# Kernel optimization log

Measured on AMD Instinct MI355X. Metric: run time of the kernel, lower is better.

Reference implementation:

```python
import jax, jax.numpy as jnp
import numpy as np
from jax import lax

MASK_ID = 0  # sequence_mask pad token

def setup_inputs() -> dict:
    key = jax.random.key(0)
    ks = jax.random.split(key, 7)
    B, T, V, E, U_, O = 256, 128, 10000, 256, 1024, 1024
    return {
        "sequences": jax.random.randint(ks[0], (B, T), 0, V),
        "emb_table": jax.random.normal(ks[1], (V, E), jnp.float32) * 0.02,
        "W": jax.random.normal(ks[2], (E, 4 * U_), jnp.float32) * (1.0 / np.sqrt(E)),
        "U": jax.random.normal(ks[3], (U_, 4 * U_), jnp.float32) * (1.0 / np.sqrt(U_)),
        "b": jnp.zeros((4 * U_,), jnp.float32),
        "fc_W": jax.random.normal(ks[4], (U_, O), jnp.float32) * (1.0 / np.sqrt(U_)),
        "fc_b": jnp.zeros((O,), jnp.float32),
    }

def reference(sequences, emb_table, W, U, b, fc_W, fc_b):
    B, T = sequences.shape
    units = U.shape[0]
    # sequence_length_fn: count of non-pad tokens per row
    lengths = jnp.sum(sequences != MASK_ID, axis=1)  # [B]
    x = emb_table[sequences]                          # [B,T,E]
    # precompute input-to-gate contribution (fuses gate matmuls across time)
    x_gates = jnp.einsum('bte,eg->btg', x, W) + b     # [B,T,4U]
    valid = (jnp.arange(T)[:, None] < lengths[None, :])  # [T,B]

    def step(carry, inp):
        h, c = carry
        xg, v = inp                                   # [B,4U], [B]
        z = xg + h @ U
        i, f, g, o = jnp.split(z, 4, axis=-1)         # keras gate order i,f,c,o
        i = jax.nn.sigmoid(i)
        f = jax.nn.sigmoid(f)
        o = jax.nn.sigmoid(o)
        g = jnp.tanh(g)
        c_new = f * c + i * g
        h_new = o * jnp.tanh(c_new)
        vm = v[:, None]
        # dynamic_rnn: zero output past length, carry state through
        h_out = jnp.where(vm, h_new, 0.0)
        return (jnp.where(vm, h_new, h), jnp.where(vm, c_new, c)), h_out

    init = (jnp.zeros((B, units), x.dtype), jnp.zeros((B, units), x.dtype))
    _, outs = lax.scan(step, init, (jnp.swapaxes(x_gates, 0, 1), valid))
    outputs = jnp.swapaxes(outs, 0, 1)                # [B,T,U]
    return outputs @ fc_W + fc_b                      # [B,T,O]
```

## Files before the change

kernel.cpp:

```cpp
#include <hip/hip_runtime.h>

typedef short bf16x8 __attribute__((ext_vector_type(8)));
typedef float f32x4  __attribute__((ext_vector_type(4)));
typedef int   i32x4  __attribute__((ext_vector_type(4)));

#define DEVINL __device__ __forceinline__

static constexpr size_t SZ_WIM  = 4096ull * 512 * 2;
static constexpr size_t SZ_FCW  = 1024ull * 2048 * 2;
static constexpr size_t SZ_UIM  = 8388608;
static constexpr size_t SZ_EBI  = 10000ull * 512 * 2;
static constexpr size_t SZ_HH   = 33ull * 524288;
static constexpr size_t SZ_CB   = 1048576;
static constexpr size_t SZ_LEN  = 4096;
static constexpr size_t SZ_DIAG = 2048;

DEVINL unsigned short bf16rn(float x){
  unsigned u = __float_as_uint(x);
  unsigned r = (u + 0x7fffu + ((u >> 16) & 1u)) >> 16;
  return (unsigned short)r;
}
DEVINL unsigned short bf16lo(float x){
  unsigned ub = __float_as_uint(x);
  return bf16rn(x - __uint_as_float(ub & 0xffff0000u));
}
DEVINL float sigm(float x){ return 1.f / (1.f + __expf(-x)); }
DEVINL float tanhfast(float x){
  float xc = fminf(15.f, fmaxf(-15.f, x));
  float e = __expf(2.f * xc);
  return (e - 1.f) / (e + 1.f);
}
DEVINL void gl_lds16(const void* g, void* l){
  __builtin_amdgcn_global_load_lds(
      (const __attribute__((address_space(1))) unsigned*)g,
      (__attribute__((address_space(3))) unsigned*)l, 16, 0, 0);
}
DEVINL int hslot(int t){ return t % 33; }

__global__ void __launch_bounds__(256) probe_fill(float* __restrict__ out, int n, float v)
{
  int i = blockIdx.x * 256 + threadIdx.x;
  if (i < n) out[i] = (i == 0) ? v : 0.f;
}

__global__ void __launch_bounds__(64) diag_check(const int* __restrict__ prog,
                                                 float* __restrict__ out)
{
  if (threadIdx.x == 0){
    int miss = 0;
    for (int i = 7; i >= 1; i--) if (prog[i] == 0) miss = i;
    if (miss){
      for (int k = 0; k < 1024; k++) out[k] = 100.0f + (float)miss;
    }
  }
}

__global__ void __launch_bounds__(128) len_kernel(const int* __restrict__ seq,
                                                  int* __restrict__ len,
                                                  int* __restrict__ prog)
{
  int b = blockIdx.x, t = threadIdx.x;
  if (b == 0 && t == 0) prog[1] = 1;
  int pred = (seq[b * 128 + t] != 0) ? 1 : 0;
  unsigned long long m = __ballot(pred);
  __shared__ int cnt[2];
  if ((t & 63) == 0) cnt[t >> 6] = __popcll(m);
  __syncthreads();
  if (t == 0) len[b] = cnt[0] + cnt[1];
}

__global__ void __launch_bounds__(256) prep_split_img(
    const float* __restrict__ S, unsigned short* __restrict__ img, int N, int Ksrc,
    int* __restrict__ prog, int stage)
{
  __shared__ float tile[64][65];
  const int nt = N >> 6;
  const int bn = blockIdx.x % nt, bk = blockIdx.x / nt;
  const int tid = threadIdx.x;
  if (blockIdx.x == 0 && tid == 0) prog[stage] = 1;
  {
    const int kk = tid >> 6, n = tid & 63;
#pragma unroll 4
    for (int i = 0; i < 16; i++){
      int k = i * 4 + kk;
      tile[k][n] = S[(size_t)((bk << 6) + k) * N + (bn << 6) + n];
    }
  }
  __syncthreads();
  {
    const int n4 = tid >> 6, k = tid & 63;
#pragma unroll 4
    for (int i = 0; i < 16; i++){
      int n = i * 4 + n4;
      float v = tile[k][n];
      size_t rowoff = (size_t)((bn << 6) + n) * (2 * Ksrc) + (bk << 6) + k;
      img[rowoff] = (unsigned short)(__float_as_uint(v) >> 16);
      img[rowoff + Ksrc] = bf16lo(v);
    }
  }
}

__global__ void __launch_bounds__(256) prep_emb_img(const float* __restrict__ emb,
                                                    unsigned short* __restrict__ img)
{
  const int v = blockIdx.x, t = threadIdx.x;
  float x = emb[(size_t)v * 256 + t];
  img[(size_t)v * 512 + t]       = (unsigned short)(__float_as_uint(x) >> 16);
  img[(size_t)v * 512 + 256 + t] = bf16lo(x);
}

__global__ void __launch_bounds__(256) prep_uimg(const float* __restrict__ U,
                                                 signed char* __restrict__ img,
                                                 int* __restrict__ prog)
{
  const int bid = blockIdx.x;
  const int nb = bid >> 2, nt4 = bid & 3;
  const int tid = threadIdx.x;
  if (bid == 0 && tid == 0) prog[4] = 1;
  __shared__ signed char lc[16384], ldq[16384];
  const int colbase = nt4 * 1024 + (nb << 4);
  const int kk = tid >> 4, cc = tid & 15;
#pragma unroll 4
  for (int it = 0; it < 64; it++){
    int k = it * 16 + kk;
    float v = U[(size_t)k * 4096 + colbase + cc];
    int q = (int)rintf(v * 131072.f);
    q = q > 32639 ? 32639 : (q < -32639 ? -32639 : q);
    int a = (q + 128) >> 8;
    int d = q - (a << 8);
    lc[(k << 4) + cc]  = (signed char)a;
    ldq[(k << 4) + cc] = (signed char)d;
  }
  __syncthreads();
#pragma unroll
  for (int rep = 0; rep < 4; rep++){
    int idx = rep * 256 + tid;
    int kt = idx >> 6, lane = idx & 63;
    int n = lane & 15, quad = lane >> 4;
    union { signed char b[16]; i32x4 v; } cb_, db_;
#pragma unroll
    for (int j = 0; j < 16; j++){
      int k = (kt << 6) + (quad << 4) + j;
      cb_.b[j] = lc[(k << 4) + n];
      db_.b[j] = ldq[(k << 4) + n];
    }
    size_t base = (size_t)((((nb << 2) + nt4) * 16 + kt) * 2) * 1024;
    *(i32x4*)(img + base + (size_t)lane * 16)        = cb_.v;
    *(i32x4*)(img + base + 1024 + (size_t)lane * 16) = db_.v;
  }
}

__global__ void __launch_bounds__(256) gemm_gates(
    const unsigned short* __restrict__ Aimg, const unsigned short* __restrict__ Bimg,
    const float* __restrict__ bias, float* __restrict__ D,
    const int* __restrict__ seq, int c0, int tcsh, int* __restrict__ prog)
{
  __shared__ __align__(16) char lds[16384];
  __shared__ int stok[128];
  const int tid = threadIdx.x, lane = tid & 63, wv = tid >> 6;
  const int quad = lane >> 4, nlo = lane & 15;
  const int wm = wv & 1, wn = wv >> 1;
  const int rowbase = (blockIdx.x >> 5) << 7;
  const int colbase = (blockIdx.x & 31) << 7;
  const int tcm1 = (1 << tcsh) - 1;
  if (blockIdx.x == 0 && tid == 0) prog[5] = 1;
  if (tid < 128){
    int r = rowbase + tid;
    stok[tid] = seq[((r >> tcsh) << 7) + c0 + (r & tcm1)];
  }
  __syncthreads();

  f32x4 acc[4][4];
#pragma unroll
  for (int i = 0; i < 4; i++)
#pragma unroll
    for (int j = 0; j < 4; j++) acc[i][j] = (f32x4){0.f, 0.f, 0.f, 0.f};

  const unsigned short* asrc[2]; const unsigned short* bsrc[2];
  char* adst[2]; char* bdst[2];
#pragma unroll
  for (int p = 0; p < 2; p++){
    int gidx = p * 256 + tid;
    int row = gidx >> 2, sg = gidx & 3;
    int sgs = sg ^ ((row >> 1) & 3);
    asrc[p] = Aimg + (size_t)stok[row] * 512 + sgs * 8;
    bsrc[p] = Bimg + (size_t)(colbase + row) * 512 + sgs * 8;
    adst[p] = &lds[p * 4096 + wv * 1024];
    bdst[p] = &lds[8192 + p * 4096 + wv * 1024];
  }

#pragma unroll 2
  for (int c = 0; c < 24; c++){
    int k0 = c * 32;
    int seg = (k0 >= 512) ? 2 : (k0 >= 256 ? 1 : 0);
    int acol = k0 - seg * 256;
    int aoff = (seg == 1 ? 256 : 0) + acol;
    int boff = (seg == 2 ? 256 : 0) + acol;
    __syncthreads();
#pragma unroll
    for (int p = 0; p < 2; p++){
      gl_lds16(asrc[p] + aoff, adst[p]);
      gl_lds16(bsrc[p] + boff, bdst[p]);
    }
    __syncthreads();
    bf16x8 af[4], bfr[4];
#pragma unroll
    for (int mt = 0; mt < 4; mt++){
      int r = wm * 64 + mt * 16 + nlo;
      af[mt] = *(const bf16x8*)(&lds[r * 64 + ((quad ^ ((r >> 1) & 3)) << 4)]);
    }
#pragma unroll
    for (int nt = 0; nt < 4; nt++){
      int r = wn * 64 + nt * 16 + nlo;
      bfr[nt] = *(const bf16x8*)(&lds[8192 + r * 64 + ((quad ^ ((r >> 1) & 3)) << 4)]);
    }
#pragma unroll
    for (int mt = 0; mt < 4; mt++)
#pragma unroll
      for (int nt = 0; nt < 4; nt++)
        acc[mt][nt] = __builtin_amdgcn_mfma_f32_16x16x32_bf16(af[mt], bfr[nt], acc[mt][nt], 0, 0, 0);
  }

  float bs[4];
#pragma unroll
  for (int nt = 0; nt < 4; nt++) bs[nt] = bias[colbase + wn * 64 + nt * 16 + nlo];
#pragma unroll
  for (int mt = 0; mt < 4; mt++)
#pragma unroll
    for (int nt = 0; nt < 4; nt++){
      int col = colbase + wn * 64 + nt * 16 + nlo;
#pragma unroll
      for (int r = 0; r < 4; r++){
        int row = rowbase + wm * 64 + mt * 16 + quad * 4 + r;
        D[(size_t)row * 4096 + col] = acc[mt][nt][r] + bs[nt];
      }
    }
}

__global__ void __launch_bounds__(256) gemm_out(
    const unsigned short* __restrict__ ohol, const unsigned short* __restrict__ Bimg,
    const float* __restrict__ bias, float* __restrict__ D,
    int c0, int tcsh, int* __restrict__ prog)
{
  __shared__ __align__(16) char lds[16384];
  const int tid = threadIdx.x, lane = tid & 63, wv = tid >> 6;
  const int quad = lane >> 4, nlo = lane & 15;
  const int wm = wv & 1, wn = wv >> 1;
  const int rowbase = (blockIdx.x >> 3) << 7;
  const int colbase = (blockIdx.x & 7) << 7;
  const int tcm1 = (1 << tcsh) - 1;
  if (blockIdx.x == 0 && tid == 0) prog[7] = 1;

  f32x4 acc[4][4];
#pragma unroll
  for (int i = 0; i < 4; i++)
#pragma unroll
    for (int j = 0; j < 4; j++) acc[i][j] = (f32x4){0.f, 0.f, 0.f, 0.f};

  const unsigned short* asrc[2]; const unsigned short* bsrc[2];
  char* adst[2]; char* bdst[2];
#pragma unroll
  for (int p = 0; p < 2; p++){
    int gidx = p * 256 + tid;
    int row = gidx >> 2, sg = gidx & 3;
    int sgs = sg ^ ((row >> 1) & 3);
    asrc[p] = ohol + (size_t)(rowbase + row) * 2048 + sgs * 8;
    bsrc[p] = Bimg + (size_t)(colbase + row) * 2048 + sgs * 8;
    adst[p] = &lds[p * 4096 + wv * 1024];
    bdst[p] = &lds[8192 + p * 4096 + wv * 1024];
  }

#pragma unroll 2
  for (int c = 0; c < 96; c++){
    int k0 = c * 32;
    int seg = (k0 >= 2048) ? 2 : (k0 >= 1024 ? 1 : 0);
    int acol = k0 - seg * 1024;
    int aoff = (seg == 1 ? 1024 : 0) + acol;
    int boff = (seg == 2 ? 1024 : 0) + acol;
    __syncthreads();
#pragma unroll
    for (int p = 0; p < 2; p++){
      gl_lds16(asrc[p] + aoff, adst[p]);
      gl_lds16(bsrc[p] + boff, bdst[p]);
    }
    __syncthreads();
    bf16x8 af[4], bfr[4];
#pragma unroll
    for (int mt = 0; mt < 4; mt++){
      int r = wm * 64 + mt * 16 + nlo;
      af[mt] = *(const bf16x8*)(&lds[r * 64 + ((quad ^ ((r >> 1) & 3)) << 4)]);
    }
#pragma unroll
    for (int nt = 0; nt < 4; nt++){
      int r = wn * 64 + nt * 16 + nlo;
      bfr[nt] = *(const bf16x8*)(&lds[8192 + r * 64 + ((quad ^ ((r >> 1) & 3)) << 4)]);
    }
#pragma unroll
    for (int mt = 0; mt < 4; mt++)
#pragma unroll
      for (int nt = 0; nt < 4; nt++)
        acc[mt][nt] = __builtin_amdgcn_mfma_f32_16x16x32_bf16(af[mt], bfr[nt], acc[mt][nt], 0, 0, 0);
  }

  float bs[4];
#pragma unroll
  for (int nt = 0; nt < 4; nt++) bs[nt] = bias[colbase + wn * 64 + nt * 16 + nlo];
#pragma unroll
  for (int mt = 0; mt < 4; mt++)
#pragma unroll
    for (int nt = 0; nt < 4; nt++){
      int col = colbase + wn * 64 + nt * 16 + nlo;
#pragma unroll
      for (int r = 0; r < 4; r++){
        int row = rowbase + wm * 64 + mt * 16 + quad * 4 + r;
        int drow = ((row >> tcsh) << 7) + c0 + (row & tcm1);
        D[(size_t)drow * 1024 + col] = acc[mt][nt][r] + bs[nt];
      }
    }
}

DEVINL void mbbar(int* flags, int nb, int t, int wv, int lane){
  __syncthreads();
  if (wv == 0){
    if (lane == 0)
      __hip_atomic_store(&flags[nb], t + 1, __ATOMIC_RELAXED, __HIP_MEMORY_SCOPE_AGENT);
    const int tgt = t + 1;
    for (;;){
      int v = __hip_atomic_load(&flags[lane], __ATOMIC_RELAXED, __HIP_MEMORY_SCOPE_AGENT);
      if (__ballot(v >= tgt) == ~0ull) break;
      __builtin_amdgcn_s_sleep(1);
    }
    __builtin_amdgcn_fence(__ATOMIC_ACQUIRE, "workgroup");
  }
  __syncthreads();
}

__global__ void __launch_bounds__(512, 2) lstm_rec(
    const float* __restrict__ xg,
    const signed char* __restrict__ uimg,
    const int* __restrict__ len,
    signed char* __restrict__ hh,
    float* __restrict__ cbuf,
    unsigned short* __restrict__ ohol,
    int* __restrict__ barbase,
    int* __restrict__ prog,
    int c0, int tcsh)
{
  __shared__ __align__(16) char lds[50176];
  const int tc = 1 << tcsh;
  const int wg = blockIdx.x, mb = wg >> 6, nb = wg & 63;
  const int tid = threadIdx.x, lane = tid & 63, wv = tid >> 6;
  const int quad = lane >> 4, nlo = lane & 15;
  const int mh = wv & 1, g = wv >> 1;
  int* flags = barbase + (mb << 6);
  if (wg == 0 && tid == 0) prog[6] = 1;

  const unsigned short* hh2 = (const unsigned short*)hh;

  i32x4 Bf[16][2];
#pragma unroll
  for (int kt = 0; kt < 16; kt++)
#pragma unroll
    for (int pl = 0; pl < 2; pl++){
      size_t off = (size_t)((((nb << 2) + g) * 16 + kt) * 2 + pl);
      off = (off * 64 + lane) << 4;
      Bf[kt][pl] = *(const i32x4*)(uimg + off);
    }

  const int erow = tid >> 3;
  const int ecp  = tid & 7;
  const int ecol0 = ecp << 1;
  const int ucol0 = (nb << 4) + ecol0;
  const int bglob = (mb << 6) + erow;
  const int lenr = len[bglob];
  float cst[2], hst[2];
#pragma unroll
  for (int r = 0; r < 2; r++){
    cst[r] = cbuf[(size_t)bglob * 1024 + ucol0 + r];
    unsigned short e = hh2[(size_t)hslot(c0) * 262144 + (size_t)bglob * 1024 + ucol0 + r];
    int a = (signed char)(e >> 8), b_ = (signed char)(e & 255);
    hst[r] = (float)(a * 256 + b_) * (1.0f / 32512.0f);
  }

  float4 xreg[2];
  auto load_x = [&](int s){
#pragma unroll
    for (int it = 0; it < 2; it++){
      int idx = it * 512 + tid;
      int row = idx >> 4, c4 = idx & 15;
      xreg[it] = *(const float4*)(xg + (size_t)((((mb << 6) + row) << tcsh) + s) * 4096
                                  + (c4 >> 2) * 1024 + (nb << 4) + ((c4 & 3) << 2));
    }
  };
  load_x(0);

  const int hrw = tid >> 3, hsub = tid & 7;

#pragma unroll 1
  for (int s = 0; s < tc; s++){
    const int t = c0 + s;
    const signed char* hsrc = hh + (size_t)hslot(t) * 524288 + (size_t)(mb << 6) * 2048;

    i32x4 accH[2], accM[2], accL[2];
#pragma unroll
    for (int m = 0; m < 2; m++){
      accH[m] = (i32x4){0,0,0,0};
      accM[m] = (i32x4){0,0,0,0};
      accL[m] = (i32x4){0,0,0,0};
    }

    int4 hregA[2], hregB[2];
    auto load_hto = [&](int c, int4* dst){
      const signed char* p = hsrc + (size_t)hrw * 2048 + c * 256 + hsub * 32;
      dst[0] = *(const int4*)p;
      dst[1] = *(const int4*)(p + 16);
    };
    auto write_hf = [&](const int4* src){
      unsigned r0 = (unsigned)src[0].x, r1 = (unsigned)src[0].y;
      unsigned r2 = (unsigned)src[0].z, r3 = (unsigned)src[0].w;
      unsigned r4 = (unsigned)src[1].x, r5 = (unsigned)src[1].y;
      unsigned r6 = (unsigned)src[1].z, r7 = (unsigned)src[1].w;
      i32x4 lo, hi;
      lo[0] = __builtin_amdgcn_perm(r1, r0, 0x06040200u);
      lo[1] = __builtin_amdgcn_perm(r3, r2, 0x06040200u);
      lo[2] = __builtin_amdgcn_perm(r5, r4, 0x06040200u);
      lo[3] = __builtin_amdgcn_perm(r7, r6, 0x06040200u);
      hi[0] = __builtin_amdgcn_perm(r1, r0, 0x07050301u);
      hi[1] = __builtin_amdgcn_perm(r3, r2, 0x07050301u);
      hi[2] = __builtin_amdgcn_perm(r5, r4, 0x07050301u);
      hi[3] = __builtin_amdgcn_perm(r7, r6, 0x07050301u);
      int sw = (hsub ^ (hrw & 7)) << 4;
      *(i32x4*)(&lds[hrw * 128 + sw])        = hi;
      *(i32x4*)(&lds[8192 + hrw * 128 + sw]) = lo;
    };

    load_hto(0, hregA);
    load_hto(1, hregB);

#pragma unroll
    for (int c = 0; c < 8; c++){
      __syncthreads();
      if ((c & 1) == 0) write_hf(hregA); else write_hf(hregB);
      if (c == 0){
#pragma unroll
        for (int it = 0; it < 2; it++){
          int idx = it * 512 + tid;
          int row = idx >> 4, c4 = idx & 15;
          *(float4*)(&lds[16384 + row * 256 + c4 * 16]) = xreg[it];
        }
      }
      __syncthreads();
      if (c + 2 < 8){
        if ((c & 1) == 0) load_hto(c + 2, hregA); else load_hto(c + 2, hregB);
      }
#pragma unroll
      for (int kt2 = 0; kt2 < 2; kt2++){
        const int kt = c * 2 + kt2;
        i32x4 Af[2][2];
#pragma unroll
        for (int m = 0; m < 2; m++){
          int hrow = (mh << 5) + (m << 4) + nlo;
          int sgl = ((kt2 << 2) + quad) ^ (hrow & 7);
          Af[m][0] = *(const i32x4*)(&lds[hrow * 128 + (sgl << 4)]);
          Af[m][1] = *(const i32x4*)(&lds[8192 + hrow * 128 + (sgl << 4)]);
        }
#pragma unroll
        for (int m = 0; m < 2; m++){
          accH[m] = __builtin_amdgcn_mfma_i32_16x16x64_i8(Af[m][0], Bf[kt][0], accH[m], 0, 0, 0);
          accM[m] = __builtin_amdgcn_mfma_i32_16x16x64_i8(Af[m][0], Bf[kt][1], accM[m], 0, 0, 0);
          accM[m] = __builtin_amdgcn_mfma_i32_16x16x64_i8(Af[m][1], Bf[kt][0], accM[m], 0, 0, 0);
          accL[m] = __builtin_amdgcn_mfma_i32_16x16x64_i8(Af[m][1], Bf[kt][1], accL[m], 0, 0, 0);
        }
      }
    }
    __syncthreads();

    if (s + 1 < tc) load_x(s + 1);

    const float cH = 1.0f / 65024.0f;
    const float cM = 1.0f / 16646144.0f;
    const float cL = 1.0f / 4261412864.0f;
#pragma unroll
    for (int m = 0; m < 2; m++){
#pragma unroll
      for (int r = 0; r < 4; r++){
        float z = (float)accH[m][r] * cH
                + (float)accM[m][r] * cM
                + (float)accL[m][r] * cL;
        int zrow = (mh << 5) + (m << 4) + (quad << 2) + r;
        *(float*)(&lds[32768 + (((zrow * 68) + g * 16 + nlo) << 2)]) = z;
      }
    }
    __syncthreads();

    {
      float ho16[2];
      unsigned enc2 = 0;
#pragma unroll
      for (int r = 0; r < 2; r++){
        int col = ecol0 + r;
        float zi = *(const float*)(&lds[32768 + (((erow * 68) + 0  + col) << 2)])
                 + *(const float*)(&lds[16384 + (((erow << 6) + 0  + col) << 2)]);
        float zf = *(const float*)(&lds[32768 + (((erow * 68) + 16 + col) << 2)])
                 + *(const float*)(&lds[16384 + (((erow << 6) + 16 + col) << 2)]);
        float zg = *(const float*)(&lds[32768 + (((erow * 68) + 32 + col) << 2)])
                 + *(const float*)(&lds[16384 + (((erow << 6) + 32 + col) << 2)]);
        float zo = *(const float*)(&lds[32768 + (((erow * 68) + 48 + col) << 2)])
                 + *(const float*)(&lds[16384 + (((erow << 6) + 48 + col) << 2)]);
        float iv = sigm(zi), fv = sigm(zf), ov = sigm(zo), gv = tanhfast(zg);
        float cn = fv * cst[r] + iv * gv;
        float hn = ov * tanhfast(cn);
        bool vld = (t < lenr);
        cst[r] = vld ? cn : cst[r];
        hst[r] = vld ? hn : hst[r];
        ho16[r] = vld ? hn : 0.f;
        int H = (int)rintf(hst[r] * 32512.f);
        H = H > 32512 ? 32512 : (H < -32512 ? -32512 : H);
        int a = (H + 128) >> 8;
        int b_ = H - (a << 8);
        unsigned e = (((unsigned)a & 255u) << 8) | ((unsigned)b_ & 255u);
        enc2 |= e << (r * 16);
      }
      size_t orow = ((size_t)bglob << tcsh) + s;
      unsigned hi2 = (unsigned)(__float_as_uint(ho16[0]) >> 16)
                   | ((unsigned)(__float_as_uint(ho16[1]) >> 16) << 16);
      unsigned lo2 = (unsigned)bf16lo(ho16[0]) | ((unsigned)bf16lo(ho16[1]) << 16);
      *(unsigned*)(ohol + orow * 2048 + ucol0)        = hi2;
      *(unsigned*)(ohol + orow * 2048 + 1024 + ucol0) = lo2;
      unsigned* hp = (unsigned*)(hh + (size_t)hslot(t + 1) * 524288
                                 + ((size_t)bglob * 1024 + ucol0) * 2);
      unsigned old = __hip_atomic_exchange(hp, enc2, __ATOMIC_RELAXED,
                                           __HIP_MEMORY_SCOPE_AGENT);
      asm volatile("" :: "v"(old));
    }
    mbbar(flags, nb, t, wv, lane);
  }

#pragma unroll
  for (int r = 0; r < 2; r++)
    cbuf[(size_t)bglob * 1024 + ucol0 + r] = cst[r];
}

extern "C" void kernel_launch(void* const* d_in, const int* in_sizes, int n_in,
                              void* d_out, int out_size, void* d_ws, size_t ws_size,
                              hipStream_t stream)
{
  const int*   seq = (const int*)  d_in[0];
  const float* emb = (const float*)d_in[1];
  const float* Wm  = (const float*)d_in[2];
  const float* Um  = (const float*)d_in[3];
  const float* bv  = (const float*)d_in[4];
  const float* fcW = (const float*)d_in[5];
  const float* fcb = (const float*)d_in[6];
  float* out = (float*)d_out;
  char* ws = (char*)d_ws;

  hipMemsetAsync(d_out, 0x42, 256, stream);

  size_t off = 0;
  unsigned short* wim = (unsigned short*)(ws + off); off += SZ_WIM;
  unsigned short* fcw = (unsigned short*)(ws + off); off += SZ_FCW;
  signed char*    uim = (signed char*)(ws + off);    off += SZ_UIM;
  unsigned short* ebi = (unsigned short*)(ws + off); off += SZ_EBI;
  signed char*    hh  = (signed char*)(ws + off);    off += SZ_HH;
  float*          cb  = (float*)(ws + off);          off += SZ_CB;
  int*            len = (int*)(ws + off);            off += SZ_LEN;
  int*            diag= (int*)(ws + off);            off += SZ_DIAG;
  const size_t fixed = off;

  int tcsh = -1;
  for (int s = 5; s >= 0; s--)
    if (ws && fixed + (5242880ull << s) <= ws_size){ tcsh = s; break; }

  if (tcsh < 0){
    probe_fill<<<(out_size + 255) / 256, 256, 0, stream>>>(
        out, out_size, 1000.0f + (float)(ws_size >> 20));
    return;
  }
  const int tc = 1 << tcsh;

  float*          xgc  = (float*)(ws + fixed);
  unsigned short* ohol = (unsigned short*)(ws + fixed + (size_t)tc * 4194304);

  hipMemsetAsync(diag, 0, SZ_DIAG, stream);
  hipMemsetAsync(hh, 0, 524288, stream);
  hipMemsetAsync(cb, 0, SZ_CB, stream);

  int* prog = diag;
  int* barbase = diag + 64;

  len_kernel<<<256, 128, 0, stream>>>(seq, len, prog);
  prep_split_img<<<256, 256, 0, stream>>>(Wm, wim, 4096, 256, prog, 2);
  prep_split_img<<<256, 256, 0, stream>>>(fcW, fcw, 1024, 1024, prog, 3);
  prep_emb_img<<<10000, 256, 0, stream>>>(emb, ebi);
  prep_uimg<<<256, 256, 0, stream>>>(Um, uim, prog);

  for (int c0 = 0; c0 < 128; c0 += tc){
    gemm_gates<<<dim3((2 * tc) * 32), 256, 0, stream>>>(ebi, wim, bv, xgc, seq, c0, tcsh, prog);
    lstm_rec<<<dim3(256), 512, 0, stream>>>(xgc, uim, len, hh, cb, ohol, barbase, prog, c0, tcsh);
    gemm_out<<<dim3((2 * tc) * 8), 256, 0, stream>>>(ohol, fcw, fcb, out, c0, tcsh, prog);
  }

  diag_check<<<1, 64, 0, stream>>>(prog, out);
}
```

Baseline: 2.117 ms.

## Overlap next-chunk gate GEMM and previous-chunk output GEMM with recurrence

Merges the input-gate GEMM for the next time chunk and the output projection for the previous chunk into the recurrent kernel launch as extra workgroups. Gate pre-activations and hidden-output staging buffers are double-buffered so the three stages of adjacent chunks can run at once. The recurrent workgroups raise their wave priority to limit slowdown from the co-scheduled GEMM blocks. The aim is to hide GEMM time behind the latency-bound sequential recurrence and to cut kernel launches. The trade-offs are doubled workspace per chunk, which may force smaller chunks, and contention for CUs and memory bandwidth that could slow the barrier-synchronised recurrence.

```diff
diff --git a/kernel.cpp b/kernel.cpp
--- a/kernel.cpp
+++ b/kernel.cpp
@@ -335,7 +335,178 @@
   __syncthreads();
 }
 
-__global__ void __launch_bounds__(512, 2) lstm_rec(
+DEVINL void gates_body(char* ldsAll, int* stok2, int pairIdx,
+    const unsigned short* Aimg, const unsigned short* Bimg,
+    const float* bias, float* D, const int* seq, int c0g, int tcsh)
+{
+  const int tid = threadIdx.x;
+  const int half = tid >> 8, t8 = tid & 255;
+  const int lane = t8 & 63, wv = t8 >> 6;
+  const int quad = lane >> 4, nlo = lane & 15;
+  const int wm = wv & 1, wn = wv >> 1;
+  const int tile = pairIdx * 2 + half;
+  const int rowbase = (tile >> 5) << 7;
+  const int colbase = (tile & 31) << 7;
+  const int tcm1 = (1 << tcsh) - 1;
+  char* lds = ldsAll + half * 16384;
+  int* stok = stok2 + half * 128;
+  if (t8 < 128){
+    int r = rowbase + t8;
+    stok[t8] = seq[((r >> tcsh) << 7) + c0g + (r & tcm1)];
+  }
+  __syncthreads();
+
+  f32x4 acc[4][4];
+#pragma unroll
+  for (int i = 0; i < 4; i++)
+#pragma unroll
+    for (int j = 0; j < 4; j++) acc[i][j] = (f32x4){0.f, 0.f, 0.f, 0.f};
+
+  const unsigned short* asrc[2]; const unsigned short* bsrc[2];
+  char* adst[2]; char* bdst[2];
+#pragma unroll
+  for (int p = 0; p < 2; p++){
+    int gidx = p * 256 + t8;
+    int row = gidx >> 2, sg = gidx & 3;
+    int sgs = sg ^ ((row >> 1) & 3);
+    asrc[p] = Aimg + (size_t)stok[row] * 512 + sgs * 8;
+    bsrc[p] = Bimg + (size_t)(colbase + row) * 512 + sgs * 8;
+    adst[p] = &lds[p * 4096 + wv * 1024];
+    bdst[p] = &lds[8192 + p * 4096 + wv * 1024];
+  }
+
+#pragma unroll 2
+  for (int c = 0; c < 24; c++){
+    int k0 = c * 32;
+    int seg = (k0 >= 512) ? 2 : (k0 >= 256 ? 1 : 0);
+    int acol = k0 - seg * 256;
+    int aoff = (seg == 1 ? 256 : 0) + acol;
+    int boff = (seg == 2 ? 256 : 0) + acol;
+    __syncthreads();
+#pragma unroll
+    for (int p = 0; p < 2; p++){
+      gl_lds16(asrc[p] + aoff, adst[p]);
+      gl_lds16(bsrc[p] + boff, bdst[p]);
+    }
+    __syncthreads();
+    bf16x8 af[4], bfr[4];
+#pragma unroll
+    for (int mt = 0; mt < 4; mt++){
+      int r = wm * 64 + mt * 16 + nlo;
+      af[mt] = *(const bf16x8*)(&lds[r * 64 + ((quad ^ ((r >> 1) & 3)) << 4)]);
+    }
+#pragma unroll
+    for (int nt = 0; nt < 4; nt++){
+      int r = wn * 64 + nt * 16 + nlo;
+      bfr[nt] = *(const bf16x8*)(&lds[8192 + r * 64 + ((quad ^ ((r >> 1) & 3)) << 4)]);
+    }
+#pragma unroll
+    for (int mt = 0; mt < 4; mt++)
+#pragma unroll
+      for (int nt = 0; nt < 4; nt++)
+        acc[mt][nt] = __builtin_amdgcn_mfma_f32_16x16x32_bf16(af[mt], bfr[nt], acc[mt][nt], 0, 0, 0);
+  }
+
+  float bs[4];
+#pragma unroll
+  for (int nt = 0; nt < 4; nt++) bs[nt] = bias[colbase + wn * 64 + nt * 16 + nlo];
+#pragma unroll
+  for (int mt = 0; mt < 4; mt++)
+#pragma unroll
+    for (int nt = 0; nt < 4; nt++){
+      int col = colbase + wn * 64 + nt * 16 + nlo;
+#pragma unroll
+      for (int r = 0; r < 4; r++){
+        int row = rowbase + wm * 64 + mt * 16 + quad * 4 + r;
+        D[(size_t)row * 4096 + col] = acc[mt][nt][r] + bs[nt];
+      }
+    }
+}
+
+DEVINL void out_body(char* ldsAll, int pairIdx,
+    const unsigned short* ohol, const unsigned short* Bimg,
+    const float* bias, float* D, int c0o, int tcsh)
+{
+  const int tid = threadIdx.x;
+  const int half = tid >> 8, t8 = tid & 255;
+  const int lane = t8 & 63, wv = t8 >> 6;
+  const int quad = lane >> 4, nlo = lane & 15;
+  const int wm = wv & 1, wn = wv >> 1;
+  const int tile = pairIdx * 2 + half;
+  const int rowbase = (tile >> 3) << 7;
+  const int colbase = (tile & 7) << 7;
+  const int tcm1 = (1 << tcsh) - 1;
+  char* lds = ldsAll + half * 16384;
+
+  f32x4 acc[4][4];
+#pragma unroll
+  for (int i = 0; i < 4; i++)
+#pragma unroll
+    for (int j = 0; j < 4; j++) acc[i][j] = (f32x4){0.f, 0.f, 0.f, 0.f};
+
+  const unsigned short* asrc[2]; const unsigned short* bsrc[2];
+  char* adst[2]; char* bdst[2];
+#pragma unroll
+  for (int p = 0; p < 2; p++){
+    int gidx = p * 256 + t8;
+    int row = gidx >> 2, sg = gidx & 3;
+    int sgs = sg ^ ((row >> 1) & 3);
+    asrc[p] = ohol + (size_t)(rowbase + row) * 2048 + sgs * 8;
+    bsrc[p] = Bimg + (size_t)(colbase + row) * 2048 + sgs * 8;
+    adst[p] = &lds[p * 4096 + wv * 1024];
+    bdst[p] = &lds[8192 + p * 4096 + wv * 1024];
+  }
+
+#pragma unroll 2
+  for (int c = 0; c < 96; c++){
+    int k0 = c * 32;
+    int seg = (k0 >= 2048) ? 2 : (k0 >= 1024 ? 1 : 0);
+    int acol = k0 - seg * 1024;
+    int aoff = (seg == 1 ? 1024 : 0) + acol;
+    int boff = (seg == 2 ? 1024 : 0) + acol;
+    __syncthreads();
+#pragma unroll
+    for (int p = 0; p < 2; p++){
+      gl_lds16(asrc[p] + aoff, adst[p]);
+      gl_lds16(bsrc[p] + boff, bdst[p]);
+    }
+    __syncthreads();
+    bf16x8 af[4], bfr[4];
+#pragma unroll
+    for (int mt = 0; mt < 4; mt++){
+      int r = wm * 64 + mt * 16 + nlo;
+      af[mt] = *(const bf16x8*)(&lds[r * 64 + ((quad ^ ((r >> 1) & 3)) << 4)]);
+    }
+#pragma unroll
+    for (int nt = 0; nt < 4; nt++){
+      int r = wn * 64 + nt * 16 + nlo;
+      bfr[nt] = *(const bf16x8*)(&lds[8192 + r * 64 + ((quad ^ ((r >> 1) & 3)) << 4)]);
+    }
+#pragma unroll
+    for (int mt = 0; mt < 4; mt++)
+#pragma unroll
+      for (int nt = 0; nt < 4; nt++)
+        acc[mt][nt] = __builtin_amdgcn_mfma_f32_16x16x32_bf16(af[mt], bfr[nt], acc[mt][nt], 0, 0, 0);
+  }
+
+  float bs[4];
+#pragma unroll
+  for (int nt = 0; nt < 4; nt++) bs[nt] = bias[colbase + wn * 64 + nt * 16 + nlo];
+#pragma unroll
+  for (int mt = 0; mt < 4; mt++)
+#pragma unroll
+    for (int nt = 0; nt < 4; nt++){
+      int col = colbase + wn * 64 + nt * 16 + nlo;
+#pragma unroll
+      for (int r = 0; r < 4; r++){
+        int row = rowbase + wm * 64 + mt * 16 + quad * 4 + r;
+        int drow = ((row >> tcsh) << 7) + c0o + (row & tcm1);
+        D[(size_t)drow * 1024 + col] = acc[mt][nt][r] + bs[nt];
+      }
+    }
+}
+
+__global__ void __launch_bounds__(512, 2) fused_step(
     const float* __restrict__ xg,
     const signed char* __restrict__ uimg,
     const int* __restrict__ len,
@@ -344,11 +515,32 @@
     unsigned short* __restrict__ ohol,
     int* __restrict__ barbase,
     int* __restrict__ prog,
-    int c0, int tcsh)
+    int c0, int tcsh,
+    const unsigned short* __restrict__ ebi, const unsigned short* __restrict__ wim,
+    const float* __restrict__ bv, float* __restrict__ xg_nxt,
+    const int* __restrict__ seq,
+    const unsigned short* __restrict__ ohol_prv, const unsigned short* __restrict__ fcw,
+    const float* __restrict__ fcb, float* __restrict__ outp,
+    int ngg)
 {
   __shared__ __align__(16) char lds[50176];
+  __shared__ int stok2[256];
+  const int bid = blockIdx.x;
+
+  if (bid >= 256){
+    if (bid < 256 + ngg){
+      gates_body(lds, stok2, bid - 256, ebi, wim, bv, xg_nxt, seq,
+                 c0 + (1 << tcsh), tcsh);
+    } else {
+      out_body(lds, bid - 256 - ngg, ohol_prv, fcw, fcb, outp,
+               c0 - (1 << tcsh), tcsh);
+    }
+    return;
+  }
+
+  __builtin_amdgcn_s_setprio(1);
   const int tc = 1 << tcsh;
-  const int wg = blockIdx.x, mb = wg >> 6, nb = wg & 63;
+  const int wg = bid, mb = wg >> 6, nb = wg & 63;
   const int tid = threadIdx.x, lane = tid & 63, wv = tid >> 6;
   const int quad = lane >> 4, nlo = lane & 15;
   const int mh = wv & 1, g = wv >> 1;
@@ -570,7 +762,7 @@
 
   int tcsh = -1;
   for (int s = 5; s >= 0; s--)
-    if (ws && fixed + (5242880ull << s) <= ws_size){ tcsh = s; break; }
+    if (ws && fixed + (10485760ull << s) <= ws_size){ tcsh = s; break; }
 
   if (tcsh < 0){
     probe_fill<<<(out_size + 255) / 256, 256, 0, stream>>>(
@@ -578,9 +770,13 @@
     return;
   }
   const int tc = 1 << tcsh;
-
-  float*          xgc  = (float*)(ws + fixed);
-  unsigned short* ohol = (unsigned short*)(ws + fixed + (size_t)tc * 4194304);
+  const int nc = 128 >> tcsh;
+
+  float*          xgA = (float*)(ws + fixed);
+  float*          xgB = (float*)(ws + fixed + (size_t)tc * 4194304);
+  unsigned short* ohA = (unsigned short*)(ws + fixed + (size_t)tc * 8388608);
+  unsigned short* ohB = (unsigned short*)(ws + fixed + (size_t)tc * 8388608
+                                          + (size_t)tc * 1048576);
 
   hipMemsetAsync(diag, 0, SZ_DIAG, stream);
   hipMemsetAsync(hh, 0, 524288, stream);
@@ -595,11 +791,24 @@
   prep_emb_img<<<10000, 256, 0, stream>>>(emb, ebi);
   prep_uimg<<<256, 256, 0, stream>>>(Um, uim, prog);
 
-  for (int c0 = 0; c0 < 128; c0 += tc){
-    gemm_gates<<<dim3((2 * tc) * 32), 256, 0, stream>>>(ebi, wim, bv, xgc, seq, c0, tcsh, prog);
-    lstm_rec<<<dim3(256), 512, 0, stream>>>(xgc, uim, len, hh, cb, ohol, barbase, prog, c0, tcsh);
-    gemm_out<<<dim3((2 * tc) * 8), 256, 0, stream>>>(ohol, fcw, fcb, out, c0, tcsh, prog);
-  }
+  gemm_gates<<<dim3((2 * tc) * 32), 256, 0, stream>>>(ebi, wim, bv, xgA, seq, 0, tcsh, prog);
+
+  for (int k = 0; k < nc; k++){
+    int c0 = k << tcsh;
+    float*          xg_cur = (k & 1) ? xgB : xgA;
+    float*          xg_nxt = (k & 1) ? xgA : xgB;
+    unsigned short* oh_cur = (k & 1) ? ohB : ohA;
+    unsigned short* oh_prv = (k & 1) ? ohA : ohB;
+    int ngg = (k + 1 < nc) ? (tc * 32) : 0;
+    int ngo = (k >= 1)     ? (tc * 8)  : 0;
+    fused_step<<<dim3(256 + ngg + ngo), 512, 0, stream>>>(
+        xg_cur, uim, len, hh, cb, oh_cur, barbase, prog, c0, tcsh,
+        ebi, wim, bv, xg_nxt, seq,
+        oh_prv, fcw, fcb, out, ngg);
+  }
+
+  gemm_out<<<dim3((2 * tc) * 8), 256, 0, stream>>>(
+      ((nc - 1) & 1) ? ohB : ohA, fcw, fcb, out, 128 - tc, tcsh, prog);
 
   diag_check<<<1, 64, 0, stream>>>(prog, out);
 }
```

Result: slower. 2.319 ms (+9.6%).
